# Kernel optimization log

Measured on AMD Instinct MI355X. Metric: run time of the kernel, lower is better.

## Reference

```python
import jax, jax.numpy as jnp
import numpy as np

B, L, D_MODEL, D_INNER, P = 4, 16384, 256, 512, 64  # P = d_state, conj_sym=False
STEP_RESCALE = 1.0


def setup_inputs() -> dict:
    key = jax.random.key(0)
    ks = jax.random.split(key, 11)
    # projections (bias=False)
    W_in = jax.random.normal(ks[0], (D_MODEL, 2 * D_INNER), jnp.float32) * (1.0 / np.sqrt(D_MODEL))
    W_out = jax.random.normal(ks[1], (D_INNER, D_MODEL), jnp.float32) * (1.0 / np.sqrt(D_INNER))
    # diagonal SSM params: Lambda = A_real + i*A_imag, HiPPO-like (negative real part)
    A_real = -0.5 * jnp.ones((P,), jnp.float32) - jax.random.uniform(ks[2], (P,), jnp.float32)
    A_imag = jnp.pi * jnp.arange(P, dtype=jnp.float32) * (jax.random.uniform(ks[3], (P,), jnp.float32) * 0.1 + 0.95)
    B_re = jax.random.normal(ks[4], (P, D_INNER), jnp.float32) * (1.0 / np.sqrt(P))
    B_im = jax.random.normal(ks[5], (P, D_INNER), jnp.float32) * (1.0 / np.sqrt(P))
    C_re = jax.random.normal(ks[6], (D_INNER, P), jnp.float32) * (1.0 / np.sqrt(D_INNER))
    C_im = jax.random.normal(ks[7], (D_INNER, P), jnp.float32) * (1.0 / np.sqrt(D_INNER))
    D = jax.random.normal(ks[8], (D_INNER,), jnp.float32)
    # dt ~ loguniform[dt_min, dt_max]; inv_dt = softplus^{-1}(dt) = dt + log(-expm1(-dt))
    dt = jnp.exp(jax.random.uniform(ks[9], (P,), jnp.float32) * (np.log(0.1) - np.log(0.001)) + np.log(0.001))
    dt = jnp.clip(dt, 1e-4, None)
    inv_dt = dt + jnp.log(-jnp.expm1(-dt))
    x = jax.random.normal(ks[10], (B, L, D_MODEL), jnp.float32)
    return {"x": x, "W_in": W_in, "W_out": W_out, "A_real": A_real, "A_imag": A_imag,
            "B_re": B_re, "B_im": B_im, "C_re": C_re, "C_im": C_im, "D": D, "inv_dt": inv_dt}


def _binop(e1, e2):
    a1, b1 = e1
    a2, b2 = e2
    return a2 * a1, a2 * b1 + b2


def reference(x, W_in, W_out, A_real, A_imag, B_re, B_im, C_re, C_im, D, inv_dt):
    # in_proj + gate split
    x_and_res = x @ W_in                       # (b, l, 2*d_inner)
    u, res = jnp.split(x_and_res, 2, axis=-1)
    u = jax.nn.silu(u)                         # (b, l, d_inner)
    # bilinear discretization of diagonal SSM
    A = A_real + 1j * A_imag                   # (P,)
    dt = STEP_RESCALE * jax.nn.softplus(inv_dt)  # (P,)
    BL = 1.0 / (1.0 - (dt / 2.0) * A)
    dA = BL * (1.0 + (dt / 2.0) * A)           # (P,)
    dB = (BL * dt)[:, None] * (B_re + 1j * B_im)  # (P, d_inner)
    # drive: Bu_t = dB @ u_t
    Bu = u.astype(dA.dtype) @ dB.T             # (b, l, P) complex
    # parallel (associative) scan of h_t = dA*h_{t-1} + Bu_t  (h_0 = 0)
    elems = (jnp.broadcast_to(dA, Bu.shape), Bu)
    _, h = jax.lax.associative_scan(_binop, elems, axis=1)  # (b, l, P)
    C = C_re + 1j * C_im                       # (d_inner, P)
    y = jnp.real(h @ C.T) + D * u              # (b, l, d_inner), + skip D*u
    y = y * jax.nn.silu(res)
    return y @ W_out                           # (b, l, d_model)
```

## Files before the change

### kernel.cpp

```cpp
#include <hip/hip_runtime.h>
#include <math.h>

#define NTOK 65536
#define LSEQ 16384
#define GCH 64
#define NCH 256

typedef __attribute__((ext_vector_type(8))) short short8v;
typedef __attribute__((ext_vector_type(4))) float f32x4;
typedef unsigned short u16;

__device__ __forceinline__ u16 f2bf(float f) {
  unsigned u = __float_as_uint(f);
  return (u16)((u + 0x7FFFu + ((u >> 16) & 1u)) >> 16);
}
__device__ __forceinline__ float bf2f(u16 b) {
  return __uint_as_float(((unsigned)b) << 16);
}
__device__ __forceinline__ unsigned cvtpk_bf16(float lo, float hi) {
  unsigned r;
  asm("v_cvt_pk_bf16_f32 %0, %1, %2" : "=v"(r) : "v"(lo), "v"(hi));
  return r;
}
__device__ __forceinline__ float silu_f(float v) {
  return v * __builtin_amdgcn_rcpf(1.f + __expf(-v));
}
__device__ __forceinline__ void gld16(const u16* g, u16* l) {
  __builtin_amdgcn_global_load_lds((const __attribute__((address_space(1))) void*)g,
                                   (__attribute__((address_space(3))) void*)l, 16, 0, 0);
}

#define WAITV2 asm volatile("s_waitcnt vmcnt(2) lgkmcnt(0)" ::: "memory")
#define WAITV1 asm volatile("s_waitcnt vmcnt(1) lgkmcnt(0)" ::: "memory")
#define WAITV0 asm volatile("s_waitcnt vmcnt(0) lgkmcnt(0)" ::: "memory")
#define BARRAW asm volatile("s_barrier" ::: "memory")

__global__ void setup_scalar_k(const float* __restrict__ A_real, const float* __restrict__ A_imag,
                               const float* __restrict__ inv_dt,
                               float2* __restrict__ dAf, float2* __restrict__ fvec,
                               float2* __restrict__ powt) {
  int p = threadIdx.x;
  if (p >= 64) return;
  double ar = (double)A_real[p], ai = (double)A_imag[p];
  double dt = log1p(exp((double)inv_dt[p]));
  double zr = 0.5 * dt * ar, zi = 0.5 * dt * ai;
  double d1r = 1.0 - zr;
  double den = d1r * d1r + zi * zi;
  double blr = d1r / den, bli = zi / den;
  double nr = 1.0 + zr, ni = zi;
  double dar = blr * nr - bli * ni;
  double dai = blr * ni + bli * nr;
  dAf[p] = make_float2((float)dar, (float)dai);
  fvec[p] = make_float2((float)(blr * dt), (float)(bli * dt));
  double cr = 1.0, ci = 0.0;
  for (int k = 0; k <= GCH; ++k) {
    powt[p * (GCH + 1) + k] = make_float2((float)cr, (float)ci);
    double t = cr * dar - ci * dai;
    ci = cr * dai + ci * dar;
    cr = t;
  }
}

__global__ void setup_tables_k(const float* __restrict__ B_re, const float* __restrict__ B_im,
                               const float* __restrict__ C_re, const float* __restrict__ C_im,
                               const float* __restrict__ W_in, const float* __restrict__ W_out,
                               const float2* __restrict__ fvec,
                               u16* __restrict__ WinT, u16* __restrict__ dBn,
                               u16* __restrict__ Ccb, u16* __restrict__ WoutT) {
  int idx = blockIdx.x * blockDim.x + threadIdx.x;
  int stride = gridDim.x * blockDim.x;
  for (int i = idx; i < 1024 * 256; i += stride) {
    int n = i >> 8, k = i & 255;
    WinT[i] = f2bf(W_in[k * 1024 + n]);
  }
  for (int i = idx; i < 128 * 512; i += stride) {
    int p = i >> 9, d = i & 511;
    float2 f = fvec[p & 63];
    float br = B_re[(p & 63) * 512 + d], bi = B_im[(p & 63) * 512 + d];
    float v = (p < 64) ? (f.x * br - f.y * bi) : (f.x * bi + f.y * br);
    dBn[i] = f2bf(v);
  }
  for (int i = idx; i < 512 * 128; i += stride) {
    int d = i >> 7, k = i & 127;
    float v = (k < 64) ? C_re[d * 64 + k] : -C_im[d * 64 + (k - 64)];
    Ccb[i] = f2bf(v);
  }
  for (int i = idx; i < 256 * 512; i += stride) {
    int n = i >> 9, k = i & 511;
    WoutT[i] = f2bf(W_out[k * 256 + n]);
  }
}

template<int MODE, int LOG_NBX, int KDIM, int AFP32>
__global__ __launch_bounds__(1024) void mgemm2(
    const void* __restrict__ Ain, const u16* __restrict__ Bt,
    void* __restrict__ C0, void* __restrict__ C1,
    const float* __restrict__ Dvec) {
  constexpr int NBUF = AFP32 ? 2 : 3;
  constexpr int NT = KDIM / 32;
  __shared__ u16 As[NBUF][128 * 32];
  __shared__ u16 Bs[NBUF][256 * 32];
  const int tid = threadIdx.x;
  const int w = tid >> 6, l = tid & 63;
  const int wm = w >> 3, wn = w & 7;
  const bool isA = (w < 8);

  const int lin = blockIdx.x;
  const int cpx = gridDim.x >> 3;
  const int swz = (lin & 7) * cpx + (lin >> 3);
  const int n0 = (swz & ((1 << LOG_NBX) - 1)) * 256;
  const int m0 = (swz >> LOG_NBX) * 128;

  f32x4 acc[4][2] = {};

  const int fr = l & 15;
  const int kgs = (((l >> 4) ^ (l >> 1)) & 3) * 8;
  const int sr = l >> 2;
  const int scl = l & 3;
  const int scs = scl ^ ((l >> 3) & 3);

  const float* gA32 = nullptr;
  const u16* gA16 = nullptr;
  const u16* gB = nullptr;
  if (isA) {
    int row = w * 16 + sr;
    if (AFP32) gA32 = (const float*)Ain + (size_t)(m0 + row) * KDIM + scl * 8;
    else       gA16 = (const u16*)Ain + (size_t)(m0 + row) * KDIM + scs * 8;
  } else {
    int row = (w - 8) * 16 + sr;
    gB = Bt + (size_t)(n0 + row) * KDIM + scs * 8;
  }

  float4 ra0, ra1;
  auto loadA = [&](int k0) {
    ra0 = *(const float4*)(gA32 + k0);
    ra1 = *(const float4*)(gA32 + k0 + 4);
  };
  auto writeA = [&](int buf) {
    unsigned q0 = cvtpk_bf16(ra0.x, ra0.y), q1 = cvtpk_bf16(ra0.z, ra0.w);
    unsigned q2 = cvtpk_bf16(ra1.x, ra1.y), q3 = cvtpk_bf16(ra1.z, ra1.w);
    int row = w * 16 + sr;
    *(uint4*)&As[buf][row * 32 + scs * 8] = make_uint4(q0, q1, q2, q3);
  };
  auto stageB = [&](int buf, int k0) {
    gld16(gB + k0, &Bs[buf][(w - 8) * 512]);
    gld16(gB + k0 + (size_t)128 * KDIM, &Bs[buf][(w - 8) * 512 + 4096]);
  };
  auto stageA16 = [&](int buf, int k0) {
    gld16(gA16 + k0, &As[buf][w * 512]);
  };
  auto compute = [&](int buf) {
    short8v af[4], bfr[2];
#pragma unroll
    for (int mi = 0; mi < 4; ++mi)
      af[mi] = *(const short8v*)&As[buf][(wm * 64 + mi * 16 + fr) * 32 + kgs];
#pragma unroll
    for (int ni = 0; ni < 2; ++ni)
      bfr[ni] = *(const short8v*)&Bs[buf][(wn * 32 + ni * 16 + fr) * 32 + kgs];
#pragma unroll
    for (int mi = 0; mi < 4; ++mi)
#pragma unroll
      for (int ni = 0; ni < 2; ++ni)
        acc[mi][ni] = __builtin_amdgcn_mfma_f32_16x16x32_bf16(af[mi], bfr[ni], acc[mi][ni], 0, 0, 0);
  };

  if (AFP32) {
    if (isA) {
      loadA(0);
      asm volatile("s_waitcnt vmcnt(0)" ::: "memory");
      writeA(0);
    } else {
      stageB(0, 0);
    }
    __syncthreads();
#pragma unroll
    for (int t = 0; t < NT; ++t) {
      if (t + 1 < NT) {
        if (isA) loadA((t + 1) * 32);
        else     stageB((t + 1) & 1, (t + 1) * 32);
      }
      compute(t & 1);
      if (t + 1 < NT && isA) {
        asm volatile("s_waitcnt vmcnt(0)" ::: "memory");
        writeA((t + 1) & 1);
      }
      __syncthreads();
    }
  } else {
    if (isA) stageA16(0, 0); else stageB(0, 0);
    if (isA) stageA16(1, 32); else stageB(1, 32);
#pragma unroll
    for (int t = 0; t < NT; ++t) {
      if (t + 1 < NT) { if (isA) { WAITV1; } else { WAITV2; } } else { WAITV0; }
      BARRAW;
      if (t + 2 < NT) {
        if (isA) stageA16((t + 2) % 3, (t + 2) * 32);
        else     stageB((t + 2) % 3, (t + 2) * 32);
      }
      compute(t % 3);
    }
  }

  const int rbase = (l >> 4) * 4;
#pragma unroll
  for (int mi = 0; mi < 4; ++mi) {
#pragma unroll
    for (int ni = 0; ni < 2; ++ni) {
      int gr0 = m0 + wm * 64 + mi * 16 + rbase;
      int gc = n0 + wn * 32 + ni * 16 + fr;
      if (MODE == 0) {
        float s0 = silu_f(acc[mi][ni][0]);
        float s1 = silu_f(acc[mi][ni][1]);
        float s2 = silu_f(acc[mi][ni][2]);
        float s3 = silu_f(acc[mi][ni][3]);
        unsigned p01 = cvtpk_bf16(s0, s1);
        unsigned p23 = cvtpk_bf16(s2, s3);
        u16* Cw = (n0 < 512) ? (u16*)C0 : (u16*)C1;
        int col = gc - ((n0 < 512) ? 0 : 512);
        Cw[(size_t)(gr0 + 0) * 512 + col] = (u16)p01;
        Cw[(size_t)(gr0 + 1) * 512 + col] = (u16)(p01 >> 16);
        Cw[(size_t)(gr0 + 2) * 512 + col] = (u16)p23;
        Cw[(size_t)(gr0 + 3) * 512 + col] = (u16)(p23 >> 16);
      } else if (MODE == 2) {
        float g[4];
#pragma unroll
        for (int j = 0; j < 4; ++j) {
          size_t r = (size_t)(gr0 + j);
          float uu = bf2f(((const u16*)C0)[r * 512 + gc]);
          float sr2 = bf2f(((const u16*)C1)[r * 512 + gc]);
          g[j] = (acc[mi][ni][j] + Dvec[gc] * uu) * sr2;
        }
        unsigned p01 = cvtpk_bf16(g[0], g[1]);
        unsigned p23 = cvtpk_bf16(g[2], g[3]);
        ((u16*)C1)[(size_t)(gr0 + 0) * 512 + gc] = (u16)p01;
        ((u16*)C1)[(size_t)(gr0 + 1) * 512 + gc] = (u16)(p01 >> 16);
        ((u16*)C1)[(size_t)(gr0 + 2) * 512 + gc] = (u16)p23;
        ((u16*)C1)[(size_t)(gr0 + 3) * 512 + gc] = (u16)(p23 >> 16);
      } else {
#pragma unroll
        for (int j = 0; j < 4; ++j)
          ((float*)C0)[(size_t)(gr0 + j) * 256 + gc] = acc[mi][ni][j];
      }
    }
  }
}

__global__ __launch_bounds__(512) void k2_bu_carry(
    const u16* __restrict__ A, const u16* __restrict__ Bt,
    float* __restrict__ Bu, float* __restrict__ carr, float* __restrict__ carr2,
    const float2* __restrict__ dAf, const float2* __restrict__ powt) {
  constexpr int KDIM = 512;
  constexpr int NT = KDIM / 32;
  __shared__ u16 As[3][128 * 32];
  __shared__ u16 Bs[3][128 * 32];
  const int tid = threadIdx.x;
  const int w = tid >> 6, l = tid & 63;
  const int wm = w >> 2, wn = w & 3;

  const int lin = blockIdx.x;
  const int cpx = gridDim.x >> 3;
  const int swz = (lin & 7) * cpx + (lin >> 3);
  const int m0 = swz * 128;

  f32x4 acc[4][2] = {};

  const int lr = l >> 2;
  const int sc = (l & 3) ^ ((l >> 3) & 3);
  const u16* gA = A + (size_t)(m0 + w * 16 + lr) * KDIM + sc * 8;
  const u16* gB = Bt + (size_t)(w * 16 + lr) * KDIM + sc * 8;

  const int fr = l & 15;
  const int kgs = (((l >> 4) ^ (l >> 1)) & 3) * 8;

  auto stage = [&](int buf, int k0) {
    gld16(gA + k0, &As[buf][w * 512]);
    gld16(gB + k0, &Bs[buf][w * 512]);
  };
  auto compute = [&](int buf) {
    short8v af[4], bfr[2];
#pragma unroll
    for (int mi = 0; mi < 4; ++mi)
      af[mi] = *(const short8v*)&As[buf][(wm * 64 + mi * 16 + fr) * 32 + kgs];
#pragma unroll
    for (int ni = 0; ni < 2; ++ni)
      bfr[ni] = *(const short8v*)&Bs[buf][(wn * 32 + ni * 16 + fr) * 32 + kgs];
#pragma unroll
    for (int mi = 0; mi < 4; ++mi)
#pragma unroll
      for (int ni = 0; ni < 2; ++ni)
        acc[mi][ni] = __builtin_amdgcn_mfma_f32_16x16x32_bf16(af[mi], bfr[ni], acc[mi][ni], 0, 0, 0);
  };

  stage(0, 0);
  stage(1, 32);
#pragma unroll
  for (int t = 0; t < NT; ++t) {
    if (t + 1 < NT) { WAITV2; } else { WAITV0; }
    BARRAW;
    if (t + 2 < NT) stage((t + 2) % 3, (t + 2) * 32);
    compute(t % 3);
  }

  const int lg = l >> 4;
  const int rbase = lg * 4;
#pragma unroll
  for (int mi = 0; mi < 4; ++mi)
#pragma unroll
    for (int ni = 0; ni < 2; ++ni) {
      int gr0 = m0 + wm * 64 + mi * 16 + rbase;
      int gc = wn * 32 + ni * 16 + fr;
#pragma unroll
      for (int j = 0; j < 4; ++j)
        Bu[(size_t)(gr0 + j) * 128 + gc] = acc[mi][ni][j];
    }
  const int cu = (m0 >> 6) + wm;
#pragma unroll
  for (int ni = 0; ni < 2; ++ni) {
    int gc = wn * 32 + ni * 16 + fr;
    int p = gc & 63;
    float2 dA = dAf[p];
    float sre = 0.f, sim = 0.f;
#pragma unroll
    for (int mi = 0; mi < 4; ++mi) {
      float tr = 0.f, ti = 0.f;
#pragma unroll
      for (int j = 0; j < 4; ++j) {
        float v = acc[mi][ni][j];
        float nr = fmaf(dA.x, tr, fmaf(-dA.y, ti, v));
        float nim = fmaf(dA.x, ti, dA.y * tr);
        tr = nr; ti = nim;
      }
      float2 wg = powt[p * (GCH + 1) + 60 - lg * 4 - 16 * mi];
      sre = fmaf(wg.x, tr, fmaf(-wg.y, ti, sre));
      sim = fmaf(wg.x, ti, fmaf(wg.y, tr, sim));
    }
    sre += __shfl_xor(sre, 16); sim += __shfl_xor(sim, 16);
    sre += __shfl_xor(sre, 32); sim += __shfl_xor(sim, 32);
    if (lg == 0) {
      size_t crow = (size_t)cu * 128;
      if (gc < 64) { carr[crow + p] = sre;  carr[crow + 64 + p] = sim; }
      else         { carr2[crow + p] = -sim; carr2[crow + 64 + p] = sre; }
    }
  }
}

__global__ void scan_carry_k(const float* __restrict__ carr, const float* __restrict__ carr2,
                             float* __restrict__ offc, const float2* __restrict__ powt) {
  int b = threadIdx.x >> 6;
  int p = threadIdx.x & 63;
  float2 dAG = powt[p * (GCH + 1) + GCH];
  float rr = 0.f, ri = 0.f;
  for (int c0 = 0; c0 < NCH; c0 += 8) {
    float er[8], ei[8];
#pragma unroll
    for (int j = 0; j < 8; ++j) {
      size_t crow = (size_t)(b * NCH + c0 + j) * 128;
      er[j] = carr[crow + p] + carr2[crow + p];
      ei[j] = carr[crow + 64 + p] + carr2[crow + 64 + p];
    }
#pragma unroll
    for (int j = 0; j < 8; ++j) {
      size_t orow = (size_t)(b * NCH + c0 + j) * 128;
      offc[orow + p] = rr;
      offc[orow + 64 + p] = ri;
      float nr = fmaf(dAG.x, rr, fmaf(-dAG.y, ri, er[j]));
      float ni = fmaf(dAG.x, ri, fmaf(dAG.y, rr, ei[j]));
      rr = nr; ri = ni;
    }
  }
}

__global__ __launch_bounds__(256) void scan_emit_k(const float* __restrict__ Bu,
                                                   const float* __restrict__ offc,
                                                   u16* __restrict__ hb,
                                                   const float2* __restrict__ dAf) {
  int unit = blockIdx.x * 4 + (threadIdx.x >> 6);
  int p = threadIdx.x & 63;
  int b = unit >> 8, c = unit & 255;
  float2 dA = dAf[p];
  size_t base = ((size_t)b * LSEQ + (size_t)c * GCH) * 128;
  float hr = offc[(size_t)unit * 128 + p];
  float hi = offc[(size_t)unit * 128 + 64 + p];
  for (int i0 = 0; i0 < GCH; i0 += 8) {
    float br[8], bi[8];
#pragma unroll
    for (int j = 0; j < 8; ++j) {
      br[j] = Bu[base + (size_t)(i0 + j) * 128 + p];
      bi[j] = Bu[base + (size_t)(i0 + j) * 128 + 64 + p];
    }
#pragma unroll
    for (int j = 0; j < 8; ++j) {
      float nr = fmaf(dA.x, hr, fmaf(-dA.y, hi, br[j]));
      float ni = fmaf(dA.x, hi, fmaf(dA.y, hr, bi[j]));
      hr = nr; hi = ni;
      hb[base + (size_t)(i0 + j) * 128 + p] = f2bf(hr);
      hb[base + (size_t)(i0 + j) * 128 + 64 + p] = f2bf(hi);
    }
  }
}

extern "C" void kernel_launch(void* const* d_in, const int* in_sizes, int n_in,
                              void* d_out, int out_size, void* d_ws, size_t ws_size,
                              hipStream_t stream) {
  const float* x      = (const float*)d_in[0];
  const float* W_in   = (const float*)d_in[1];
  const float* W_out  = (const float*)d_in[2];
  const float* A_real = (const float*)d_in[3];
  const float* A_imag = (const float*)d_in[4];
  const float* B_re   = (const float*)d_in[5];
  const float* B_im   = (const float*)d_in[6];
  const float* C_re   = (const float*)d_in[7];
  const float* C_im   = (const float*)d_in[8];
  const float* Dv     = (const float*)d_in[9];
  const float* inv_dt = (const float*)d_in[10];

  u16* u_bf  = (u16*)d_ws;
  u16* sr_bf = u_bf + (size_t)NTOK * 512;
  u16* h_bf  = sr_bf + (size_t)NTOK * 512;
  u16* WinT  = h_bf + (size_t)NTOK * 128;
  u16* dBn   = WinT + 1024 * 256;
  u16* Ccb   = dBn + 128 * 512;
  u16* WoutT = Ccb + 512 * 128;

  float* O    = (float*)d_out;
  float* Bu   = O;
  float* offc = O + 8388608;
  float* carr = O + 8519680;
  float* car2 = O + 8650752;
  float2* powt = (float2*)(O + 8781824);
  float2* dAf  = (float2*)(O + 8790144);
  float2* fvec = (float2*)(O + 8790272);

  setup_scalar_k<<<1, 64, 0, stream>>>(A_real, A_imag, inv_dt, dAf, fvec, powt);
  setup_tables_k<<<256, 256, 0, stream>>>(B_re, B_im, C_re, C_im, W_in, W_out, fvec,
                                          WinT, dBn, Ccb, WoutT);

  mgemm2<0, 2, 256, 1><<<2048, 1024, 0, stream>>>(x, WinT, u_bf, sr_bf, nullptr);
  k2_bu_carry<<<512, 512, 0, stream>>>(u_bf, dBn, Bu, carr, car2, dAf, powt);
  scan_carry_k<<<1, 256, 0, stream>>>(carr, car2, offc, powt);
  scan_emit_k<<<256, 256, 0, stream>>>(Bu, offc, h_bf, dAf);
  mgemm2<2, 1, 128, 0><<<1024, 1024, 0, stream>>>(h_bf, Ccb, u_bf, sr_bf, Dv);
  mgemm2<3, 0, 512, 0><<<512, 1024, 0, stream>>>(sr_bf, WoutT, O, nullptr, nullptr);
}
```

Baseline: 239.2 us.

## Replace fp32-input projection GEMM with dedicated deeper-pipelined 512-thread kernel

The first GEMM (x @ W_in with an fp32 A operand) moves out of the generic mgemm2 template into a new kernel, k1_fused. It uses 128x128 tiles with 512 threads, and every wave loads both A and B instead of splitting waves into loader roles. The fp32 A tile is prefetched two steps ahead into alternating register sets via inline-asm global loads, and B is triple-buffered through direct-to-LDS loads. Explicit vmcnt waits and sched barriers replace __syncthreads, so the fp32 loads and bf16 conversion overlap with the MFMAs. The risks are the hand-counted waitcnt correctness and the higher register use from the extra prefetch buffers.

```diff
diff --git a/kernel.cpp b/kernel.cpp
--- a/kernel.cpp
+++ b/kernel.cpp
@@ -30,6 +30,12 @@
                                    (__attribute__((address_space(3))) void*)l, 16, 0, 0);
 }
 
+#define GLOAD(dst, ptr) \
+  asm volatile("global_load_dwordx4 %0, %1, off" : "=&v"(dst) : "v"(ptr) : "memory")
+#define SCHEDB __builtin_amdgcn_sched_barrier(0)
+#define WAITV4 asm volatile("s_waitcnt vmcnt(4)" ::: "memory")
+#define WAITV1a asm volatile("s_waitcnt vmcnt(1)" ::: "memory")
+#define WAITV3L asm volatile("s_waitcnt vmcnt(3) lgkmcnt(0)" ::: "memory")
 #define WAITV2 asm volatile("s_waitcnt vmcnt(2) lgkmcnt(0)" ::: "memory")
 #define WAITV1 asm volatile("s_waitcnt vmcnt(1) lgkmcnt(0)" ::: "memory")
 #define WAITV0 asm volatile("s_waitcnt vmcnt(0) lgkmcnt(0)" ::: "memory")
@@ -91,15 +97,113 @@
   }
 }
 
-template<int MODE, int LOG_NBX, int KDIM, int AFP32>
+__global__ __launch_bounds__(512) void k1_fused(
+    const float* __restrict__ X, const u16* __restrict__ WinT,
+    u16* __restrict__ u_bf, u16* __restrict__ sr_bf) {
+  constexpr int KDIM = 256, NT = 8;
+  __shared__ u16 As[2][128 * 32];
+  __shared__ u16 Bs[3][128 * 32];
+  const int tid = threadIdx.x;
+  const int w = tid >> 6, l = tid & 63;
+  const int wm = w >> 2, wn = w & 3;
+
+  const int lin = blockIdx.x;
+  const int cpx = gridDim.x >> 3;
+  const int swz = (lin & 7) * cpx + (lin >> 3);
+  const int n0 = (swz & 7) * 128;
+  const int m0 = (swz >> 3) * 128;
+
+  f32x4 acc[4][2] = {};
+  const int fr = l & 15;
+  const int kgs = (((l >> 4) ^ (l >> 1)) & 3) * 8;
+  const int sr = l >> 2;
+  const int scl = l & 3;
+  const int scs = scl ^ ((l >> 3) & 3);
+  const int arow = w * 16 + sr;
+  const float* gA = X + (size_t)(m0 + arow) * KDIM + scl * 8;
+  const u16* gB = WinT + (size_t)(n0 + w * 16 + sr) * KDIM + scs * 8;
+
+  float4 rp0, rp1, rq0, rq1;
+
+  auto writeA = [&](int buf, const float4& a0, const float4& a1) {
+    unsigned q0 = cvtpk_bf16(a0.x, a0.y), q1 = cvtpk_bf16(a0.z, a0.w);
+    unsigned q2 = cvtpk_bf16(a1.x, a1.y), q3 = cvtpk_bf16(a1.z, a1.w);
+    *(uint4*)&As[buf][arow * 32 + scs * 8] = make_uint4(q0, q1, q2, q3);
+  };
+  auto stageB = [&](int buf, int t) { gld16(gB + t * 32, &Bs[buf][w * 512]); };
+  auto compute = [&](int ab, int bb) {
+    short8v af[4], bfr[2];
+#pragma unroll
+    for (int mi = 0; mi < 4; ++mi)
+      af[mi] = *(const short8v*)&As[ab][(wm * 64 + mi * 16 + fr) * 32 + kgs];
+#pragma unroll
+    for (int ni = 0; ni < 2; ++ni)
+      bfr[ni] = *(const short8v*)&Bs[bb][(wn * 32 + ni * 16 + fr) * 32 + kgs];
+#pragma unroll
+    for (int mi = 0; mi < 4; ++mi)
+#pragma unroll
+      for (int ni = 0; ni < 2; ++ni)
+        acc[mi][ni] = __builtin_amdgcn_mfma_f32_16x16x32_bf16(af[mi], bfr[ni], acc[mi][ni], 0, 0, 0);
+  };
+
+  GLOAD(rp0, gA);          GLOAD(rp1, gA + 4);
+  stageB(0, 0);
+  GLOAD(rq0, gA + 32);     GLOAD(rq1, gA + 36);
+  stageB(1, 1);
+  WAITV4; SCHEDB;
+  writeA(0, rp0, rp1);
+  WAITV3L;
+  BARRAW;
+
+#pragma unroll
+  for (int t = 0; t < NT; ++t) {
+    if (t + 2 < NT) {
+      if ((t & 1) == 0) { GLOAD(rp0, gA + (t + 2) * 32); GLOAD(rp1, gA + (t + 2) * 32 + 4); }
+      else              { GLOAD(rq0, gA + (t + 2) * 32); GLOAD(rq1, gA + (t + 2) * 32 + 4); }
+      stageB((t + 2) % 3, t + 2);
+    }
+    compute(t & 1, t % 3);
+    if (t + 1 < NT) {
+      if (t + 2 < NT) { WAITV4; } else { WAITV1a; }
+      SCHEDB;
+      if (((t + 1) & 1) == 0) writeA(0, rp0, rp1);
+      else                    writeA(1, rq0, rq1);
+      if (t + 2 < NT) { WAITV3L; } else { WAITV0; }
+      BARRAW;
+    }
+  }
+
+  const int rbase = (l >> 4) * 4;
+#pragma unroll
+  for (int mi = 0; mi < 4; ++mi) {
+#pragma unroll
+    for (int ni = 0; ni < 2; ++ni) {
+      int gr0 = m0 + wm * 64 + mi * 16 + rbase;
+      int gc = n0 + wn * 32 + ni * 16 + fr;
+      float s0 = silu_f(acc[mi][ni][0]);
+      float s1 = silu_f(acc[mi][ni][1]);
+      float s2 = silu_f(acc[mi][ni][2]);
+      float s3 = silu_f(acc[mi][ni][3]);
+      unsigned p01 = cvtpk_bf16(s0, s1);
+      unsigned p23 = cvtpk_bf16(s2, s3);
+      u16* Cw = (n0 < 512) ? u_bf : sr_bf;
+      int col = gc - ((n0 < 512) ? 0 : 512);
+      Cw[(size_t)(gr0 + 0) * 512 + col] = (u16)p01;
+      Cw[(size_t)(gr0 + 1) * 512 + col] = (u16)(p01 >> 16);
+      Cw[(size_t)(gr0 + 2) * 512 + col] = (u16)p23;
+      Cw[(size_t)(gr0 + 3) * 512 + col] = (u16)(p23 >> 16);
+    }
+  }
+}
+
+template<int MODE, int LOG_NBX, int KDIM>
 __global__ __launch_bounds__(1024) void mgemm2(
-    const void* __restrict__ Ain, const u16* __restrict__ Bt,
+    const u16* __restrict__ Ain, const u16* __restrict__ Bt,
     void* __restrict__ C0, void* __restrict__ C1,
     const float* __restrict__ Dvec) {
-  constexpr int NBUF = AFP32 ? 2 : 3;
   constexpr int NT = KDIM / 32;
-  __shared__ u16 As[NBUF][128 * 32];
-  __shared__ u16 Bs[NBUF][256 * 32];
+  __shared__ u16 As[3][128 * 32];
+  __shared__ u16 Bs[3][256 * 32];
   const int tid = threadIdx.x;
   const int w = tid >> 6, l = tid & 63;
   const int wm = w >> 3, wn = w & 7;
@@ -116,38 +220,20 @@
   const int fr = l & 15;
   const int kgs = (((l >> 4) ^ (l >> 1)) & 3) * 8;
   const int sr = l >> 2;
-  const int scl = l & 3;
-  const int scs = scl ^ ((l >> 3) & 3);
-
-  const float* gA32 = nullptr;
-  const u16* gA16 = nullptr;
+  const int scs = (l & 3) ^ ((l >> 3) & 3);
+
+  const u16* gA = nullptr;
   const u16* gB = nullptr;
-  if (isA) {
-    int row = w * 16 + sr;
-    if (AFP32) gA32 = (const float*)Ain + (size_t)(m0 + row) * KDIM + scl * 8;
-    else       gA16 = (const u16*)Ain + (size_t)(m0 + row) * KDIM + scs * 8;
-  } else {
-    int row = (w - 8) * 16 + sr;
-    gB = Bt + (size_t)(n0 + row) * KDIM + scs * 8;
-  }
-
-  float4 ra0, ra1;
-  auto loadA = [&](int k0) {
-    ra0 = *(const float4*)(gA32 + k0);
-    ra1 = *(const float4*)(gA32 + k0 + 4);
-  };
-  auto writeA = [&](int buf) {
-    unsigned q0 = cvtpk_bf16(ra0.x, ra0.y), q1 = cvtpk_bf16(ra0.z, ra0.w);
-    unsigned q2 = cvtpk_bf16(ra1.x, ra1.y), q3 = cvtpk_bf16(ra1.z, ra1.w);
-    int row = w * 16 + sr;
-    *(uint4*)&As[buf][row * 32 + scs * 8] = make_uint4(q0, q1, q2, q3);
-  };
-  auto stageB = [&](int buf, int k0) {
-    gld16(gB + k0, &Bs[buf][(w - 8) * 512]);
-    gld16(gB + k0 + (size_t)128 * KDIM, &Bs[buf][(w - 8) * 512 + 4096]);
-  };
-  auto stageA16 = [&](int buf, int k0) {
-    gld16(gA16 + k0, &As[buf][w * 512]);
+  if (isA) gA = Ain + (size_t)(m0 + w * 16 + sr) * KDIM + scs * 8;
+  else     gB = Bt + (size_t)(n0 + (w - 8) * 16 + sr) * KDIM + scs * 8;
+
+  auto stage = [&](int buf, int k0) {
+    if (isA) {
+      gld16(gA + k0, &As[buf][w * 512]);
+    } else {
+      gld16(gB + k0, &Bs[buf][(w - 8) * 512]);
+      gld16(gB + k0 + (size_t)128 * KDIM, &Bs[buf][(w - 8) * 512 + 4096]);
+    }
   };
   auto compute = [&](int buf) {
     short8v af[4], bfr[2];
@@ -164,41 +250,14 @@
         acc[mi][ni] = __builtin_amdgcn_mfma_f32_16x16x32_bf16(af[mi], bfr[ni], acc[mi][ni], 0, 0, 0);
   };
 
-  if (AFP32) {
-    if (isA) {
-      loadA(0);
-      asm volatile("s_waitcnt vmcnt(0)" ::: "memory");
-      writeA(0);
-    } else {
-      stageB(0, 0);
-    }
-    __syncthreads();
-#pragma unroll
-    for (int t = 0; t < NT; ++t) {
-      if (t + 1 < NT) {
-        if (isA) loadA((t + 1) * 32);
-        else     stageB((t + 1) & 1, (t + 1) * 32);
-      }
-      compute(t & 1);
-      if (t + 1 < NT && isA) {
-        asm volatile("s_waitcnt vmcnt(0)" ::: "memory");
-        writeA((t + 1) & 1);
-      }
-      __syncthreads();
-    }
-  } else {
-    if (isA) stageA16(0, 0); else stageB(0, 0);
-    if (isA) stageA16(1, 32); else stageB(1, 32);
-#pragma unroll
-    for (int t = 0; t < NT; ++t) {
-      if (t + 1 < NT) { if (isA) { WAITV1; } else { WAITV2; } } else { WAITV0; }
-      BARRAW;
-      if (t + 2 < NT) {
-        if (isA) stageA16((t + 2) % 3, (t + 2) * 32);
-        else     stageB((t + 2) % 3, (t + 2) * 32);
-      }
-      compute(t % 3);
-    }
+  stage(0, 0);
+  stage(1, 32);
+#pragma unroll
+  for (int t = 0; t < NT; ++t) {
+    if (t + 1 < NT) { if (isA) { WAITV1; } else { WAITV2; } } else { WAITV0; }
+    BARRAW;
+    if (t + 2 < NT) stage((t + 2) % 3, (t + 2) * 32);
+    compute(t % 3);
   }
 
   const int rbase = (l >> 4) * 4;
@@ -208,20 +267,7 @@
     for (int ni = 0; ni < 2; ++ni) {
       int gr0 = m0 + wm * 64 + mi * 16 + rbase;
       int gc = n0 + wn * 32 + ni * 16 + fr;
-      if (MODE == 0) {
-        float s0 = silu_f(acc[mi][ni][0]);
-        float s1 = silu_f(acc[mi][ni][1]);
-        float s2 = silu_f(acc[mi][ni][2]);
-        float s3 = silu_f(acc[mi][ni][3]);
-        unsigned p01 = cvtpk_bf16(s0, s1);
-        unsigned p23 = cvtpk_bf16(s2, s3);
-        u16* Cw = (n0 < 512) ? (u16*)C0 : (u16*)C1;
-        int col = gc - ((n0 < 512) ? 0 : 512);
-        Cw[(size_t)(gr0 + 0) * 512 + col] = (u16)p01;
-        Cw[(size_t)(gr0 + 1) * 512 + col] = (u16)(p01 >> 16);
-        Cw[(size_t)(gr0 + 2) * 512 + col] = (u16)p23;
-        Cw[(size_t)(gr0 + 3) * 512 + col] = (u16)(p23 >> 16);
-      } else if (MODE == 2) {
+      if (MODE == 2) {
         float g[4];
 #pragma unroll
         for (int j = 0; j < 4; ++j) {
@@ -435,10 +481,10 @@
   setup_tables_k<<<256, 256, 0, stream>>>(B_re, B_im, C_re, C_im, W_in, W_out, fvec,
                                           WinT, dBn, Ccb, WoutT);
 
-  mgemm2<0, 2, 256, 1><<<2048, 1024, 0, stream>>>(x, WinT, u_bf, sr_bf, nullptr);
+  k1_fused<<<4096, 512, 0, stream>>>(x, WinT, u_bf, sr_bf);
   k2_bu_carry<<<512, 512, 0, stream>>>(u_bf, dBn, Bu, carr, car2, dAf, powt);
   scan_carry_k<<<1, 256, 0, stream>>>(carr, car2, offc, powt);
   scan_emit_k<<<256, 256, 0, stream>>>(Bu, offc, h_bf, dAf);
-  mgemm2<2, 1, 128, 0><<<1024, 1024, 0, stream>>>(h_bf, Ccb, u_bf, sr_bf, Dv);
-  mgemm2<3, 0, 512, 0><<<512, 1024, 0, stream>>>(sr_bf, WoutT, O, nullptr, nullptr);
-}
+  mgemm2<2, 1, 128><<<1024, 1024, 0, stream>>>(h_bf, Ccb, u_bf, sr_bf, Dv);
+  mgemm2<3, 0, 512><<<512, 1024, 0, stream>>>(sr_bf, WoutT, O, nullptr, nullptr);
+}
```

After: 223.7 us. -6.5%, faster.
